# Kernel tuning notes

Hardware: AMD Instinct MI355X
Metric: run time of the kernel (lower is better)

## Reference

```python
import jax, jax.numpy as jnp
import numpy as np

N, E = 50000, 600000
IN, H, C = 128, 8, 32
HC = H * C
LAT, OUT, NCOM = 32, 64, 30
BN_EPS = 1e-5
NEG_SLOPE = 0.2


def setup_inputs() -> dict:
    key = jax.random.key(0)
    ks = jax.random.split(key, 32)
    f32 = jnp.float32
    def rn(i, shape, s=0.05):
        return jax.random.normal(ks[i], shape, f32) * s
    inp = {
        'x': jax.random.normal(ks[0], (N, IN), f32),
        'eps': jax.random.normal(ks[1], (N, LAT), f32),
        'edge_index': jax.random.randint(ks[2], (2, E), 0, N, jnp.int32),
        # GAT layer 1 (in -> H*C)
        'gat1_W': rn(3, (IN, HC)), 'gat1_asrc': rn(4, (H, C)), 'gat1_adst': rn(5, (H, C)), 'gat1_b': jnp.zeros((HC,), f32),
        'bn1_g': jnp.ones((HC,), f32), 'bn1_b': jnp.zeros((HC,), f32),
        # GAT layer 2 (H*C -> H*C)
        'gat2_W': rn(6, (HC, HC)), 'gat2_asrc': rn(7, (H, C)), 'gat2_adst': rn(8, (H, C)), 'gat2_b': jnp.zeros((HC,), f32),
        'bn2_g': jnp.ones((HC,), f32), 'bn2_b': jnp.zeros((HC,), f32),
        # GAT layer 3 (H*C -> H*C)
        'gat3_W': rn(9, (HC, HC)), 'gat3_asrc': rn(10, (H, C)), 'gat3_adst': rn(11, (H, C)), 'gat3_b': jnp.zeros((HC,), f32),
        'bn3_g': jnp.ones((HC,), f32), 'bn3_b': jnp.zeros((HC,), f32),
        # heads
        'res_W': rn(12, (IN, HC)), 'res_b': jnp.zeros((HC,), f32),
        'mu_W': rn(13, (HC, LAT)), 'mu_b': jnp.zeros((LAT,), f32),
        'lv_W': rn(14, (HC, LAT)), 'lv_b': jnp.zeros((LAT,), f32),
        'dec_W': rn(15, (LAT, OUT)), 'dec_b': jnp.zeros((OUT,), f32),
        'aux_W': rn(16, (HC, NCOM)), 'aux_b': jnp.zeros((NCOM,), f32),
    }
    return inp


def gat_conv(x, src, dst, W, asrc, adst, b):
    # PyG GATConv (concat=True, self-loops already in src/dst, lin bias=False)
    n = x.shape[0]
    h = (x @ W).reshape(n, H, C)                      # [N,H,C]
    a_s = jnp.einsum('nhc,hc->nh', h, asrc)           # [N,H]
    a_d = jnp.einsum('nhc,hc->nh', h, adst)
    e = jax.nn.leaky_relu(a_s[src] + a_d[dst], NEG_SLOPE)  # [E,H]
    m = jax.ops.segment_max(e, dst, num_segments=n)        # per-dest softmax (stable)
    p = jnp.exp(e - m[dst])
    s = jax.ops.segment_sum(p, dst, num_segments=n)
    alpha = p / (s[dst] + 1e-16)                      # [E,H]
    out = jax.ops.segment_sum(h[src] * alpha[:, :, None], dst, num_segments=n)
    return out.reshape(n, HC) + b


def batch_norm(x, g, b):
    mu = x.mean(0)
    var = x.var(0)  # biased var, as torch BN uses for normalization
    return (x - mu) * jax.lax.rsqrt(var + BN_EPS) * g + b


def reference(x, eps, edge_index,
              gat1_W, gat1_asrc, gat1_adst, gat1_b, bn1_g, bn1_b,
              gat2_W, gat2_asrc, gat2_adst, gat2_b, bn2_g, bn2_b,
              gat3_W, gat3_asrc, gat3_adst, gat3_b, bn3_g, bn3_b,
              res_W, res_b, mu_W, mu_b, lv_W, lv_b, dec_W, dec_b, aux_W, aux_b):
    loops = jnp.arange(N, dtype=edge_index.dtype)
    src = jnp.concatenate([edge_index[0], loops])
    dst = jnp.concatenate([edge_index[1], loops])

    residual = x @ res_W + res_b
    h = jax.nn.relu(batch_norm(gat_conv(x, src, dst, gat1_W, gat1_asrc, gat1_adst, gat1_b), bn1_g, bn1_b))
    h = jax.nn.relu(batch_norm(gat_conv(h, src, dst, gat2_W, gat2_asrc, gat2_adst, gat2_b), bn2_g, bn2_b))
    h = jax.nn.relu(batch_norm(gat_conv(h, src, dst, gat3_W, gat3_asrc, gat3_adst, gat3_b), bn3_g, bn3_b))
    h = h + residual

    mu = h @ mu_W + mu_b
    logvar = h @ lv_W + lv_b
    z = mu + eps * jnp.exp(0.5 * logvar)   # reparameterize
    out = z @ dec_W + dec_b
    aux = h @ aux_W + aux_b
    return (out, mu, logvar, aux)
```

## Files before the change

### kernel.cpp

```cpp
#include <hip/hip_runtime.h>

#define N_NODES 50000
#define N_EDGES 600000
#define HC 256
#define NH 8
#define AGG_BLOCKS 1536
#define AGG_WAVES (AGG_BLOCKS * 4)

typedef short s8v __attribute__((ext_vector_type(8)));
typedef float f4v __attribute__((ext_vector_type(4)));
typedef _Float16 h4v __attribute__((ext_vector_type(4)));
typedef __attribute__((address_space(1))) const unsigned int as1_cu32;
typedef __attribute__((address_space(3))) unsigned int as3_u32;

__device__ inline ushort f2bf(float f) {
  unsigned u = __float_as_uint(f);
  unsigned r = u + 0x7FFF + ((u >> 16) & 1);
  return (ushort)(r >> 16);
}

__global__ void k_init_cnt(int* __restrict__ cnt) {
  int i = blockIdx.x * 256 + threadIdx.x;
  if (i < N_NODES) cnt[i] = 1;
}

__global__ void k_count(const int* __restrict__ dstE, int* __restrict__ cnt) {
  int e = blockIdx.x * 256 + threadIdx.x;
  if (e < N_EDGES) atomicAdd(&cnt[dstE[e]], 1);
}

__global__ void k_scan_bsum(const int* __restrict__ cnt, int* __restrict__ bsum) {
  __shared__ int sd[256];
  int i = blockIdx.x * 256 + threadIdx.x;
  sd[threadIdx.x] = (i < N_NODES) ? cnt[i] : 0;
  __syncthreads();
  for (int o = 128; o > 0; o >>= 1) {
    if (threadIdx.x < o) sd[threadIdx.x] += sd[threadIdx.x + o];
    __syncthreads();
  }
  if (threadIdx.x == 0) bsum[blockIdx.x] = sd[0];
}

__global__ void k_scan_offsets(int* __restrict__ bsum, int nb) {
  __shared__ int s[256];
  int t = threadIdx.x;
  int v = (t < nb) ? bsum[t] : 0;
  s[t] = v; __syncthreads();
  for (int o = 1; o < 256; o <<= 1) {
    int x = (t >= o) ? s[t - o] : 0;
    __syncthreads();
    s[t] += x;
    __syncthreads();
  }
  if (t < nb) bsum[t] = s[t] - v;
}

__global__ void k_scan_write(const int* __restrict__ cnt, const int* __restrict__ bsum,
                             int* __restrict__ rowptr, int* __restrict__ fillptr) {
  __shared__ int s[256];
  int t = threadIdx.x;
  int i = blockIdx.x * 256 + t;
  int v = (i < N_NODES) ? cnt[i] : 0;
  s[t] = v; __syncthreads();
  for (int o = 1; o < 256; o <<= 1) {
    int x = (t >= o) ? s[t - o] : 0;
    __syncthreads();
    s[t] += x;
    __syncthreads();
  }
  int excl = s[t] - v + bsum[blockIdx.x];
  if (i < N_NODES) {
    rowptr[i] = excl;
    fillptr[i] = excl;
    if (i == N_NODES - 1) rowptr[N_NODES] = excl + v;
  }
}

__global__ void k_fill(const int* __restrict__ srcE, const int* __restrict__ dstE,
                       int* __restrict__ fillptr, int* __restrict__ srcs) {
  int i = blockIdx.x * 256 + threadIdx.x;
  if (i < N_NODES) {
    int pos = atomicAdd(&fillptr[i], 1);
    srcs[pos] = i;
  } else if (i < N_NODES + N_EDGES) {
    int e = i - N_NODES;
    int pos = atomicAdd(&fillptr[dstE[e]], 1);
    srcs[pos] = srcE[e];
  }
}

__global__ void k_cvt_x(const float* __restrict__ X, ushort* __restrict__ Xb) {
  size_t i = ((size_t)blockIdx.x * 256 + threadIdx.x) * 4;
  float4 x4 = *(const float4*)&X[i];
  ushort4 o;
  o.x = f2bf(x4.x); o.y = f2bf(x4.y); o.z = f2bf(x4.z); o.w = f2bf(x4.w);
  *(ushort4*)&Xb[i] = o;
}

__global__ void k_cvt_wt(const float* __restrict__ W, ushort* __restrict__ Wt, int K, int Nw) {
  __shared__ ushort s[32][33];
  int tx = threadIdx.x & 31, ty = threadIdx.x >> 5;
  int k0 = blockIdx.x * 32, n0 = blockIdx.y * 32;
  for (int j = 0; j < 32; j += 8)
    s[ty + j][tx] = f2bf(W[(size_t)(k0 + ty + j) * Nw + n0 + tx]);
  __syncthreads();
  for (int j = 0; j < 32; j += 8)
    Wt[(size_t)(n0 + ty + j) * K + k0 + tx] = s[tx][ty + j];
}

__global__ void k_pack_head(const float* __restrict__ muW, const float* __restrict__ lvW,
                            const float* __restrict__ auxW, ushort* __restrict__ Wth) {
  int n = blockIdx.x;
  int k = threadIdx.x;
  float v = 0.f;
  if (n < 32) v = muW[k * 32 + n];
  else if (n < 64) v = lvW[k * 32 + (n - 32)];
  else if (n < 94) v = auxW[k * 30 + (n - 64)];
  Wth[n * 256 + k] = f2bf(v);
}

template <typename OutT>
__launch_bounds__(256)
__global__ void k_gemm_bf16(const ushort* __restrict__ A, const ushort* __restrict__ Wt,
                            const float* __restrict__ bias, OutT* __restrict__ Out,
                            int M, int K, int ldc) {
  __shared__ __align__(16) ushort As[16 * 512];
  __shared__ __align__(16) ushort Bs[16 * 512];
  int t = threadIdx.x, w = t >> 6, L = t & 63;
  int bm = blockIdx.x * 128, bn = blockIdx.y * 128;
  int lrow = L & 15, lcol = (L >> 4) * 8;

  const ushort* ga[4];
  const ushort* gb[4];
#pragma unroll
  for (int u = 0; u < 4; u++) {
    int i = w * 4 + u;
    int mt = i >> 1, ks = i & 1;
    int arow = bm + mt * 16 + lrow;
    if (arow >= M) arow = M - 1;
    ga[u] = A + (size_t)arow * K + ks * 32 + lcol;
    int brow = bn + mt * 16 + lrow;
    gb[u] = Wt + (size_t)brow * K + ks * 32 + lcol;
  }

  f4v acc[4][4];
  f4v zero = {0.f, 0.f, 0.f, 0.f};
#pragma unroll
  for (int mi = 0; mi < 4; mi++)
#pragma unroll
    for (int ni = 0; ni < 4; ni++) acc[mi][ni] = zero;

  int wm = (w >> 1) * 4;
  int wn = (w & 1) * 4;

  int nk = K >> 6;
  for (int kt = 0; kt < nk; kt++) {
#pragma unroll
    for (int u = 0; u < 4; u++) {
      int i = w * 4 + u;
      __builtin_amdgcn_global_load_lds((as1_cu32*)ga[u], (as3_u32*)&As[i * 512], 16, 0, 0);
      __builtin_amdgcn_global_load_lds((as1_cu32*)gb[u], (as3_u32*)&Bs[i * 512], 16, 0, 0);
      ga[u] += 64; gb[u] += 64;
    }
    __syncthreads();
#pragma unroll
    for (int ks = 0; ks < 2; ks++) {
      s8v af[4], bf[4];
#pragma unroll
      for (int mi = 0; mi < 4; mi++)
        af[mi] = *(const s8v*)&As[(((wm + mi) * 2 + ks) * 64 + L) * 8];
#pragma unroll
      for (int ni = 0; ni < 4; ni++)
        bf[ni] = *(const s8v*)&Bs[(((wn + ni) * 2 + ks) * 64 + L) * 8];
#pragma unroll
      for (int mi = 0; mi < 4; mi++)
#pragma unroll
        for (int ni = 0; ni < 4; ni++)
          acc[mi][ni] = __builtin_amdgcn_mfma_f32_16x16x32_bf16(af[mi], bf[ni], acc[mi][ni], 0, 0, 0);
    }
    __syncthreads();
  }
#pragma unroll
  for (int ni = 0; ni < 4; ni++) {
    int col = bn + (wn + ni) * 16 + (L & 15);
    float bb = bias ? bias[col] : 0.f;
#pragma unroll
    for (int mi = 0; mi < 4; mi++) {
      int rbase = bm + (wm + mi) * 16 + (L >> 4) * 4;
#pragma unroll
      for (int i = 0; i < 4; i++) {
        int r = rbase + i;
        if (r < M) Out[(size_t)r * ldc + col] = (OutT)(acc[mi][ni][i] + bb);
      }
    }
  }
}

__launch_bounds__(256)
__global__ void k_att(const _Float16* __restrict__ B, const float* __restrict__ asrc,
                      const float* __restrict__ adst,
                      float* __restrict__ as_, float* __restrict__ ad_) {
  int wid = (blockIdx.x * 256 + threadIdx.x) >> 6;
  int lane = threadIdx.x & 63;
  h4v x = *(const h4v*)&B[(size_t)wid * 256 + (lane << 2)];
  float4 s4 = *(const float4*)&asrc[lane << 2];
  float4 d4 = *(const float4*)&adst[lane << 2];
  float x0 = (float)x[0], x1 = (float)x[1], x2 = (float)x[2], x3 = (float)x[3];
  float vs = x0 * s4.x + x1 * s4.y + x2 * s4.z + x3 * s4.w;
  float vd = x0 * d4.x + x1 * d4.y + x2 * d4.z + x3 * d4.w;
  vs += __shfl_xor(vs, 1); vs += __shfl_xor(vs, 2); vs += __shfl_xor(vs, 4);
  vd += __shfl_xor(vd, 1); vd += __shfl_xor(vd, 2); vd += __shfl_xor(vd, 4);
  if ((lane & 7) == 0) {
    as_[wid * NH + (lane >> 3)] = vs;
    ad_[wid * NH + (lane >> 3)] = vd;
  }
}

__launch_bounds__(256)
__global__ void k_agg(const int* __restrict__ rowptr, const int* __restrict__ srcs,
                      const float* __restrict__ as_, const float* __restrict__ ad_,
                      const _Float16* __restrict__ B, const float* __restrict__ gb,
                      _Float16* __restrict__ C, float* __restrict__ part) {
  __shared__ float ss[4 * 512];
  int t = threadIdx.x;
  int w = t >> 6, lane = t & 63;
  int h = lane >> 3, j = lane & 7;
  int cb = lane << 2;
  float4 g4 = *(const float4*)&gb[cb];
  float sts0 = 0.f, sts1 = 0.f, sts2 = 0.f, sts3 = 0.f;
  float stq0 = 0.f, stq1 = 0.f, stq2 = 0.f, stq3 = 0.f;

  for (int n = blockIdx.x * 4 + w; n < N_NODES; n += AGG_WAVES) {
    int beg = rowptr[n], end = rowptr[n + 1];
    float ad_nh = ad_[n * NH + h];
    float sm = 0.f;
    for (int k = beg + j; k < end; k += 8) {
      int s = srcs[k];
      float e = as_[s * NH + h] + ad_nh;
      e = e > 0.f ? e : 0.2f * e;
      sm += __expf(e);
    }
    sm += __shfl_xor(sm, 1); sm += __shfl_xor(sm, 2); sm += __shfl_xor(sm, 4);
    float inv = 1.f / (sm + 1e-16f);
    float ac0 = 0.f, ac1 = 0.f, ac2 = 0.f, ac3 = 0.f;
    int k = beg;
    for (; k + 4 <= end; k += 4) {
      int s0 = srcs[k], s1 = srcs[k + 1], s2 = srcs[k + 2], s3 = srcs[k + 3];
      h4v b0 = *(const h4v*)&B[(size_t)s0 * 256 + cb];
      h4v b1 = *(const h4v*)&B[(size_t)s1 * 256 + cb];
      h4v b2 = *(const h4v*)&B[(size_t)s2 * 256 + cb];
      h4v b3 = *(const h4v*)&B[(size_t)s3 * 256 + cb];
      float e0 = as_[s0 * NH + h] + ad_nh; e0 = e0 > 0.f ? e0 : 0.2f * e0;
      float e1 = as_[s1 * NH + h] + ad_nh; e1 = e1 > 0.f ? e1 : 0.2f * e1;
      float e2 = as_[s2 * NH + h] + ad_nh; e2 = e2 > 0.f ? e2 : 0.2f * e2;
      float e3 = as_[s3 * NH + h] + ad_nh; e3 = e3 > 0.f ? e3 : 0.2f * e3;
      float a0 = __expf(e0) * inv, a1 = __expf(e1) * inv;
      float a2 = __expf(e2) * inv, a3 = __expf(e3) * inv;
      ac0 += a0 * (float)b0[0] + a1 * (float)b1[0] + a2 * (float)b2[0] + a3 * (float)b3[0];
      ac1 += a0 * (float)b0[1] + a1 * (float)b1[1] + a2 * (float)b2[1] + a3 * (float)b3[1];
      ac2 += a0 * (float)b0[2] + a1 * (float)b1[2] + a2 * (float)b2[2] + a3 * (float)b3[2];
      ac3 += a0 * (float)b0[3] + a1 * (float)b1[3] + a2 * (float)b2[3] + a3 * (float)b3[3];
    }
    for (; k < end; k++) {
      int s = srcs[k];
      h4v b4 = *(const h4v*)&B[(size_t)s * 256 + cb];
      float e = as_[s * NH + h] + ad_nh;
      e = e > 0.f ? e : 0.2f * e;
      float a = __expf(e) * inv;
      ac0 += a * (float)b4[0]; ac1 += a * (float)b4[1];
      ac2 += a * (float)b4[2]; ac3 += a * (float)b4[3];
    }
    float v0 = ac0 + g4.x, v1 = ac1 + g4.y, v2 = ac2 + g4.z, v3 = ac3 + g4.w;
    h4v o; o[0] = (_Float16)v0; o[1] = (_Float16)v1; o[2] = (_Float16)v2; o[3] = (_Float16)v3;
    *(h4v*)&C[(size_t)n * 256 + cb] = o;
    sts0 += v0; stq0 += v0 * v0;
    sts1 += v1; stq1 += v1 * v1;
    sts2 += v2; stq2 += v2 * v2;
    sts3 += v3; stq3 += v3 * v3;
  }
  float* sw = &ss[w * 512];
  sw[cb + 0] = sts0; sw[cb + 1] = sts1; sw[cb + 2] = sts2; sw[cb + 3] = sts3;
  sw[256 + cb + 0] = stq0; sw[256 + cb + 1] = stq1;
  sw[256 + cb + 2] = stq2; sw[256 + cb + 3] = stq3;
  __syncthreads();
  float p0 = ss[t] + ss[512 + t] + ss[1024 + t] + ss[1536 + t];
  float p1 = ss[256 + t] + ss[768 + t] + ss[1280 + t] + ss[1792 + t];
  part[(size_t)blockIdx.x * 512 + t] = p0;
  part[(size_t)blockIdx.x * 512 + 256 + t] = p1;
}

__global__ void k_bn_reduce(const float* __restrict__ part, float* __restrict__ stats) {
  int i = threadIdx.x;
  int base = blockIdx.x * (AGG_BLOCKS / 16);
  float s0 = 0.f, s1 = 0.f;
  for (int b = 0; b < AGG_BLOCKS / 16; b++) {
    s0 += part[(size_t)(base + b) * 512 + i];
    s1 += part[(size_t)(base + b) * 512 + 256 + i];
  }
  atomicAdd(&stats[i], s0);
  atomicAdd(&stats[256 + i], s1);
}

__global__ void k_bn_relu_cvt(const _Float16* __restrict__ X, const float* __restrict__ stats,
                              const float* __restrict__ g, const float* __restrict__ b,
                              const float* __restrict__ resid, ushort* __restrict__ Xb) {
  size_t i = ((size_t)blockIdx.x * 256 + threadIdx.x) * 4;
  int c = (int)(i & 255);
  const float invN = 1.f / (float)N_NODES;
  h4v x4 = *(const h4v*)&X[i];
  float4 s4 = *(const float4*)&stats[c];
  float4 q4 = *(const float4*)&stats[256 + c];
  float4 g4 = *(const float4*)&g[c];
  float4 b4 = *(const float4*)&b[c];
  float m0 = s4.x * invN, m1 = s4.y * invN, m2 = s4.z * invN, m3 = s4.w * invN;
  float v0 = ((float)x4[0] - m0) * rsqrtf(q4.x * invN - m0 * m0 + 1e-5f) * g4.x + b4.x;
  float v1 = ((float)x4[1] - m1) * rsqrtf(q4.y * invN - m1 * m1 + 1e-5f) * g4.y + b4.y;
  float v2 = ((float)x4[2] - m2) * rsqrtf(q4.z * invN - m2 * m2 + 1e-5f) * g4.z + b4.z;
  float v3 = ((float)x4[3] - m3) * rsqrtf(q4.w * invN - m3 * m3 + 1e-5f) * g4.w + b4.w;
  v0 = v0 > 0.f ? v0 : 0.f; v1 = v1 > 0.f ? v1 : 0.f;
  v2 = v2 > 0.f ? v2 : 0.f; v3 = v3 > 0.f ? v3 : 0.f;
  if (resid) {
    float4 r4 = *(const float4*)&resid[i];
    v0 += r4.x; v1 += r4.y; v2 += r4.z; v3 += r4.w;
  }
  ushort4 ob;
  ob.x = f2bf(v0); ob.y = f2bf(v1); ob.z = f2bf(v2); ob.w = f2bf(v3);
  *(ushort4*)&Xb[i] = ob;
}

__launch_bounds__(256)
__global__ void k_dec(const float* __restrict__ Hd, const float* __restrict__ eps,
                      const float* __restrict__ mub, const float* __restrict__ lvb,
                      const float* __restrict__ auxb,
                      const float* __restrict__ decW, const float* __restrict__ decb,
                      float* __restrict__ out) {
  __shared__ float wsd[2048];
  __shared__ float shz[4][32];
  int t = threadIdx.x;
  for (int i = t; i < 2048; i += 256) wsd[i] = decW[i];
  int w = t >> 6, lane = t & 63;
  int n = blockIdx.x * 4 + w;
  const float* hd = &Hd[(size_t)n * 128];
  if (lane < 32) {
    float mu = hd[lane] + mub[lane];
    float lv = hd[32 + lane] + lvb[lane];
    out[(size_t)N_NODES * 64 + (size_t)n * 32 + lane] = mu;
    out[(size_t)N_NODES * 96 + (size_t)n * 32 + lane] = lv;
    shz[w][lane] = mu + eps[(size_t)n * 32 + lane] * __expf(0.5f * lv);
  } else if (lane < 62) {
    int j = lane - 32;
    out[(size_t)N_NODES * 128 + (size_t)n * 30 + j] = hd[64 + j] + auxb[j];
  }
  __syncthreads();
  float o = decb[lane];
#pragma unroll 8
  for (int k = 0; k < 32; k++) o += shz[w][k] * wsd[k * 64 + lane];
  out[(size_t)n * 64 + lane] = o;
}

extern "C" void kernel_launch(void* const* d_in, const int* in_sizes, int n_in,
                              void* d_out, int out_size, void* d_ws, size_t ws_size,
                              hipStream_t stream) {
  (void)in_sizes; (void)n_in; (void)out_size; (void)ws_size;
  const float* x    = (const float*)d_in[0];
  const float* eps  = (const float*)d_in[1];
  const int*   ei   = (const int*)d_in[2];
  const float* gW[3]    = {(const float*)d_in[3],  (const float*)d_in[9],  (const float*)d_in[15]};
  const float* gasrc[3] = {(const float*)d_in[4],  (const float*)d_in[10], (const float*)d_in[16]};
  const float* gadst[3] = {(const float*)d_in[5],  (const float*)d_in[11], (const float*)d_in[17]};
  const float* gbias[3] = {(const float*)d_in[6],  (const float*)d_in[12], (const float*)d_in[18]};
  const float* bng[3]   = {(const float*)d_in[7],  (const float*)d_in[13], (const float*)d_in[19]};
  const float* bnb[3]   = {(const float*)d_in[8],  (const float*)d_in[14], (const float*)d_in[20]};
  const float* resW = (const float*)d_in[21];
  const float* resb = (const float*)d_in[22];
  const float* muW  = (const float*)d_in[23];
  const float* mub  = (const float*)d_in[24];
  const float* lvW  = (const float*)d_in[25];
  const float* lvb  = (const float*)d_in[26];
  const float* decW = (const float*)d_in[27];
  const float* decb = (const float*)d_in[28];
  const float* auxW = (const float*)d_in[29];
  const float* auxb = (const float*)d_in[30];
  float* out = (float*)d_out;

  char* ws = (char*)d_ws;
  size_t off = 0;
  auto alloc = [&](size_t bytes) -> void* {
    void* p = ws + off;
    off += (bytes + 255) & ~(size_t)255;
    return p;
  };
  _Float16* X0  = (_Float16*)alloc((size_t)N_NODES * HC * 2);
  _Float16* X1  = (_Float16*)alloc((size_t)N_NODES * HC * 2);
  float*  Rr    = (float*)alloc((size_t)N_NODES * HC * 4);
  float*  Hd    = (float*)alloc((size_t)N_NODES * 128 * 4);
  ushort* Xb    = (ushort*)alloc((size_t)N_NODES * HC * 2);
  float*  as_   = (float*)alloc((size_t)N_NODES * NH * 4);
  float*  ad_   = (float*)alloc((size_t)N_NODES * NH * 4);
  float*  stats = (float*)alloc(512 * 4);
  float*  part  = (float*)alloc((size_t)AGG_BLOCKS * 512 * 4);
  int* cnt      = (int*)alloc((size_t)N_NODES * 4);
  int* rowptr   = (int*)alloc((size_t)(N_NODES + 1) * 4);
  int* fillptr  = (int*)alloc((size_t)N_NODES * 4);
  int* srcs     = (int*)alloc((size_t)(N_NODES + N_EDGES) * 4);
  int* bsum     = (int*)alloc(256 * 4);
  ushort* Wt1   = (ushort*)alloc(256 * 128 * 2);
  ushort* Wt2   = (ushort*)alloc(256 * 256 * 2);
  ushort* Wt3   = (ushort*)alloc(256 * 256 * 2);
  ushort* WtR   = (ushort*)alloc(256 * 128 * 2);
  ushort* Wth   = (ushort*)alloc(128 * 256 * 2);

  const int NB = (N_NODES + 255) / 256;
  k_init_cnt<<<NB, 256, 0, stream>>>(cnt);
  k_count<<<(N_EDGES + 255) / 256, 256, 0, stream>>>(ei + N_EDGES, cnt);
  k_scan_bsum<<<NB, 256, 0, stream>>>(cnt, bsum);
  k_scan_offsets<<<1, 256, 0, stream>>>(bsum, NB);
  k_scan_write<<<NB, 256, 0, stream>>>(cnt, bsum, rowptr, fillptr);
  k_fill<<<(N_NODES + N_EDGES + 255) / 256, 256, 0, stream>>>(ei, ei + N_EDGES, fillptr, srcs);

  k_cvt_wt<<<dim3(4, 8), 256, 0, stream>>>(gW[0], Wt1, 128, 256);
  k_cvt_wt<<<dim3(8, 8), 256, 0, stream>>>(gW[1], Wt2, 256, 256);
  k_cvt_wt<<<dim3(8, 8), 256, 0, stream>>>(gW[2], Wt3, 256, 256);
  k_cvt_wt<<<dim3(4, 8), 256, 0, stream>>>(resW, WtR, 128, 256);
  k_pack_head<<<128, 256, 0, stream>>>(muW, lvW, auxW, Wth);
  k_cvt_x<<<(N_NODES * 128) / 1024, 256, 0, stream>>>(x, Xb);

  const int GM = (N_NODES + 127) / 128;
  k_gemm_bf16<float><<<dim3(GM, 2), 256, 0, stream>>>(Xb, WtR, resb, Rr, N_NODES, 128, 256);

  const ushort* Wts[3] = {Wt1, Wt2, Wt3};
  int K = 128;
  for (int L = 0; L < 3; L++) {
    k_gemm_bf16<_Float16><<<dim3(GM, 2), 256, 0, stream>>>(Xb, Wts[L], nullptr, X0, N_NODES, K, 256);
    k_att<<<N_NODES / 4, 256, 0, stream>>>(X0, gasrc[L], gadst[L], as_, ad_);
    k_agg<<<AGG_BLOCKS, 256, 0, stream>>>(rowptr, srcs, as_, ad_, X0, gbias[L], X1, part);
    hipMemsetAsync(stats, 0, 512 * 4, stream);
    k_bn_reduce<<<16, 256, 0, stream>>>(part, stats);
    k_bn_relu_cvt<<<(N_NODES * HC) / 1024, 256, 0, stream>>>(
        X1, stats, bng[L], bnb[L], (L == 2) ? Rr : nullptr, Xb);
    K = 256;
  }
  k_gemm_bf16<float><<<dim3(GM, 1), 256, 0, stream>>>(Xb, Wth, nullptr, Hd, N_NODES, 256, 128);
  k_dec<<<N_NODES / 4, 256, 0, stream>>>(Hd, eps, mub, lvb, auxb, decW, decb, out);
}
```

Baseline: 666.0 us.

## Single-pass softmax aggregation, fp16 residual/head buffers, fold stats zeroing into agg

The aggregation kernel drops its separate pass for the softmax denominator. It accumulates unnormalized exp-weighted features and the weight sum together, then divides once at the end. This halves the gather of source indices and attention scores. The residual and head GEMM outputs are now stored in fp16 instead of fp32, which halves their memory traffic. The stats memset is folded into block 0 of k_agg and the agg grid is enlarged. Zeroing stats inside k_agg while k_bn_reduce runs afterward is safe in stream order. The softmax has no max subtraction, same as before, and fp16 storage lowers the precision of the residual and head outputs.

```diff
diff --git a/kernel.cpp b/kernel.cpp
--- a/kernel.cpp
+++ b/kernel.cpp
@@ -4,7 +4,7 @@
 #define N_EDGES 600000
 #define HC 256
 #define NH 8
-#define AGG_BLOCKS 1536
+#define AGG_BLOCKS 2048
 #define AGG_WAVES (AGG_BLOCKS * 4)
 
 typedef short s8v __attribute__((ext_vector_type(8)));
@@ -220,11 +220,15 @@
 __global__ void k_agg(const int* __restrict__ rowptr, const int* __restrict__ srcs,
                       const float* __restrict__ as_, const float* __restrict__ ad_,
                       const _Float16* __restrict__ B, const float* __restrict__ gb,
-                      _Float16* __restrict__ C, float* __restrict__ part) {
+                      _Float16* __restrict__ C, float* __restrict__ part,
+                      float* __restrict__ stats) {
   __shared__ float ss[4 * 512];
   int t = threadIdx.x;
+  if (blockIdx.x == 0) {
+    stats[t] = 0.f; stats[t + 256] = 0.f;
+  }
   int w = t >> 6, lane = t & 63;
-  int h = lane >> 3, j = lane & 7;
+  int h = lane >> 3;
   int cb = lane << 2;
   float4 g4 = *(const float4*)&gb[cb];
   float sts0 = 0.f, sts1 = 0.f, sts2 = 0.f, sts3 = 0.f;
@@ -233,16 +237,7 @@
   for (int n = blockIdx.x * 4 + w; n < N_NODES; n += AGG_WAVES) {
     int beg = rowptr[n], end = rowptr[n + 1];
     float ad_nh = ad_[n * NH + h];
-    float sm = 0.f;
-    for (int k = beg + j; k < end; k += 8) {
-      int s = srcs[k];
-      float e = as_[s * NH + h] + ad_nh;
-      e = e > 0.f ? e : 0.2f * e;
-      sm += __expf(e);
-    }
-    sm += __shfl_xor(sm, 1); sm += __shfl_xor(sm, 2); sm += __shfl_xor(sm, 4);
-    float inv = 1.f / (sm + 1e-16f);
-    float ac0 = 0.f, ac1 = 0.f, ac2 = 0.f, ac3 = 0.f;
+    float ac0 = 0.f, ac1 = 0.f, ac2 = 0.f, ac3 = 0.f, wsum = 0.f;
     int k = beg;
     for (; k + 4 <= end; k += 4) {
       int s0 = srcs[k], s1 = srcs[k + 1], s2 = srcs[k + 2], s3 = srcs[k + 3];
@@ -254,23 +249,26 @@
       float e1 = as_[s1 * NH + h] + ad_nh; e1 = e1 > 0.f ? e1 : 0.2f * e1;
       float e2 = as_[s2 * NH + h] + ad_nh; e2 = e2 > 0.f ? e2 : 0.2f * e2;
       float e3 = as_[s3 * NH + h] + ad_nh; e3 = e3 > 0.f ? e3 : 0.2f * e3;
-      float a0 = __expf(e0) * inv, a1 = __expf(e1) * inv;
-      float a2 = __expf(e2) * inv, a3 = __expf(e3) * inv;
-      ac0 += a0 * (float)b0[0] + a1 * (float)b1[0] + a2 * (float)b2[0] + a3 * (float)b3[0];
-      ac1 += a0 * (float)b0[1] + a1 * (float)b1[1] + a2 * (float)b2[1] + a3 * (float)b3[1];
-      ac2 += a0 * (float)b0[2] + a1 * (float)b1[2] + a2 * (float)b2[2] + a3 * (float)b3[2];
-      ac3 += a0 * (float)b0[3] + a1 * (float)b1[3] + a2 * (float)b2[3] + a3 * (float)b3[3];
+      float p0 = __expf(e0), p1 = __expf(e1), p2 = __expf(e2), p3 = __expf(e3);
+      wsum += (p0 + p1) + (p2 + p3);
+      ac0 += p0 * (float)b0[0] + p1 * (float)b1[0] + p2 * (float)b2[0] + p3 * (float)b3[0];
+      ac1 += p0 * (float)b0[1] + p1 * (float)b1[1] + p2 * (float)b2[1] + p3 * (float)b3[1];
+      ac2 += p0 * (float)b0[2] + p1 * (float)b1[2] + p2 * (float)b2[2] + p3 * (float)b3[2];
+      ac3 += p0 * (float)b0[3] + p1 * (float)b1[3] + p2 * (float)b2[3] + p3 * (float)b3[3];
     }
     for (; k < end; k++) {
       int s = srcs[k];
       h4v b4 = *(const h4v*)&B[(size_t)s * 256 + cb];
       float e = as_[s * NH + h] + ad_nh;
       e = e > 0.f ? e : 0.2f * e;
-      float a = __expf(e) * inv;
-      ac0 += a * (float)b4[0]; ac1 += a * (float)b4[1];
-      ac2 += a * (float)b4[2]; ac3 += a * (float)b4[3];
+      float p = __expf(e);
+      wsum += p;
+      ac0 += p * (float)b4[0]; ac1 += p * (float)b4[1];
+      ac2 += p * (float)b4[2]; ac3 += p * (float)b4[3];
     }
-    float v0 = ac0 + g4.x, v1 = ac1 + g4.y, v2 = ac2 + g4.z, v3 = ac3 + g4.w;
+    float inv = 1.f / (wsum + 1e-16f);
+    float v0 = ac0 * inv + g4.x, v1 = ac1 * inv + g4.y;
+    float v2 = ac2 * inv + g4.z, v3 = ac3 * inv + g4.w;
     h4v o; o[0] = (_Float16)v0; o[1] = (_Float16)v1; o[2] = (_Float16)v2; o[3] = (_Float16)v3;
     *(h4v*)&C[(size_t)n * 256 + cb] = o;
     sts0 += v0; stq0 += v0 * v0;
@@ -303,7 +301,7 @@
 
 __global__ void k_bn_relu_cvt(const _Float16* __restrict__ X, const float* __restrict__ stats,
                               const float* __restrict__ g, const float* __restrict__ b,
-                              const float* __restrict__ resid, ushort* __restrict__ Xb) {
+                              const _Float16* __restrict__ resid, ushort* __restrict__ Xb) {
   size_t i = ((size_t)blockIdx.x * 256 + threadIdx.x) * 4;
   int c = (int)(i & 255);
   const float invN = 1.f / (float)N_NODES;
@@ -320,8 +318,8 @@
   v0 = v0 > 0.f ? v0 : 0.f; v1 = v1 > 0.f ? v1 : 0.f;
   v2 = v2 > 0.f ? v2 : 0.f; v3 = v3 > 0.f ? v3 : 0.f;
   if (resid) {
-    float4 r4 = *(const float4*)&resid[i];
-    v0 += r4.x; v1 += r4.y; v2 += r4.z; v3 += r4.w;
+    h4v r4 = *(const h4v*)&resid[i];
+    v0 += (float)r4[0]; v1 += (float)r4[1]; v2 += (float)r4[2]; v3 += (float)r4[3];
   }
   ushort4 ob;
   ob.x = f2bf(v0); ob.y = f2bf(v1); ob.z = f2bf(v2); ob.w = f2bf(v3);
@@ -329,7 +327,7 @@
 }
 
 __launch_bounds__(256)
-__global__ void k_dec(const float* __restrict__ Hd, const float* __restrict__ eps,
+__global__ void k_dec(const _Float16* __restrict__ Hd, const float* __restrict__ eps,
                       const float* __restrict__ mub, const float* __restrict__ lvb,
                       const float* __restrict__ auxb,
                       const float* __restrict__ decW, const float* __restrict__ decb,
@@ -340,16 +338,16 @@
   for (int i = t; i < 2048; i += 256) wsd[i] = decW[i];
   int w = t >> 6, lane = t & 63;
   int n = blockIdx.x * 4 + w;
-  const float* hd = &Hd[(size_t)n * 128];
+  const _Float16* hd = &Hd[(size_t)n * 128];
   if (lane < 32) {
-    float mu = hd[lane] + mub[lane];
-    float lv = hd[32 + lane] + lvb[lane];
+    float mu = (float)hd[lane] + mub[lane];
+    float lv = (float)hd[32 + lane] + lvb[lane];
     out[(size_t)N_NODES * 64 + (size_t)n * 32 + lane] = mu;
     out[(size_t)N_NODES * 96 + (size_t)n * 32 + lane] = lv;
     shz[w][lane] = mu + eps[(size_t)n * 32 + lane] * __expf(0.5f * lv);
   } else if (lane < 62) {
     int j = lane - 32;
-    out[(size_t)N_NODES * 128 + (size_t)n * 30 + j] = hd[64 + j] + auxb[j];
+    out[(size_t)N_NODES * 128 + (size_t)n * 30 + j] = (float)hd[64 + j] + auxb[j];
   }
   __syncthreads();
   float o = decb[lane];
@@ -392,8 +390,8 @@
   };
   _Float16* X0  = (_Float16*)alloc((size_t)N_NODES * HC * 2);
   _Float16* X1  = (_Float16*)alloc((size_t)N_NODES * HC * 2);
-  float*  Rr    = (float*)alloc((size_t)N_NODES * HC * 4);
-  float*  Hd    = (float*)alloc((size_t)N_NODES * 128 * 4);
+  _Float16* Rr  = (_Float16*)alloc((size_t)N_NODES * HC * 2);
+  _Float16* Hd  = (_Float16*)alloc((size_t)N_NODES * 128 * 2);
   ushort* Xb    = (ushort*)alloc((size_t)N_NODES * HC * 2);
   float*  as_   = (float*)alloc((size_t)N_NODES * NH * 4);
   float*  ad_   = (float*)alloc((size_t)N_NODES * NH * 4);
@@ -426,20 +424,19 @@
   k_cvt_x<<<(N_NODES * 128) / 1024, 256, 0, stream>>>(x, Xb);
 
   const int GM = (N_NODES + 127) / 128;
-  k_gemm_bf16<float><<<dim3(GM, 2), 256, 0, stream>>>(Xb, WtR, resb, Rr, N_NODES, 128, 256);
+  k_gemm_bf16<_Float16><<<dim3(GM, 2), 256, 0, stream>>>(Xb, WtR, resb, Rr, N_NODES, 128, 256);
 
   const ushort* Wts[3] = {Wt1, Wt2, Wt3};
   int K = 128;
   for (int L = 0; L < 3; L++) {
     k_gemm_bf16<_Float16><<<dim3(GM, 2), 256, 0, stream>>>(Xb, Wts[L], nullptr, X0, N_NODES, K, 256);
     k_att<<<N_NODES / 4, 256, 0, stream>>>(X0, gasrc[L], gadst[L], as_, ad_);
-    k_agg<<<AGG_BLOCKS, 256, 0, stream>>>(rowptr, srcs, as_, ad_, X0, gbias[L], X1, part);
-    hipMemsetAsync(stats, 0, 512 * 4, stream);
+    k_agg<<<AGG_BLOCKS, 256, 0, stream>>>(rowptr, srcs, as_, ad_, X0, gbias[L], X1, part, stats);
     k_bn_reduce<<<16, 256, 0, stream>>>(part, stats);
     k_bn_relu_cvt<<<(N_NODES * HC) / 1024, 256, 0, stream>>>(
         X1, stats, bng[L], bnb[L], (L == 2) ? Rr : nullptr, Xb);
     K = 256;
   }
-  k_gemm_bf16<float><<<dim3(GM, 1), 256, 0, stream>>>(Xb, Wth, nullptr, Hd, N_NODES, 256, 128);
+  k_gemm_bf16<_Float16><<<dim3(GM, 1), 256, 0, stream>>>(Xb, Wth, nullptr, Hd, N_NODES, 256, 128);
   k_dec<<<N_NODES / 4, 256, 0, stream>>>(Hd, eps, mub, lvb, auxb, decW, decb, out);
 }
```

Result: faster. 651.9 us (-2.1%).
